# Kernel optimization log

Hardware: AMD Instinct MI355X
Metric: run time of the kernel (lower is better)

The kernel has to match this reference:

```python
import jax, jax.numpy as jnp
import numpy as np

N_NODES = 50000
N_EDGES = 800000
F_IN = 64
F_OUT = 64
EPS = 1e-5


def setup_inputs() -> dict:
    key = jax.random.key(0)
    ks = jax.random.split(key, 6)
    x = jax.random.normal(ks[0], (N_NODES, F_IN), dtype=jnp.float32)
    edge_index = jax.random.randint(ks[1], (2, N_EDGES), 0, N_NODES, dtype=jnp.int64)
    # pre MLP: Linear(2*F_in -> F_in); post MLP: Linear(13*F_in -> F_out); lin: Linear(F_out -> F_out)
    pre_w = jax.random.normal(ks[2], (2 * F_IN, F_IN), dtype=jnp.float32) / np.sqrt(2 * F_IN)
    pre_b = jnp.zeros((F_IN,), dtype=jnp.float32)
    post_w = jax.random.normal(ks[3], (13 * F_IN, F_OUT), dtype=jnp.float32) / np.sqrt(13 * F_IN)
    post_b = jnp.zeros((F_OUT,), dtype=jnp.float32)
    lin_w = jax.random.normal(ks[4], (F_OUT, F_OUT), dtype=jnp.float32) / np.sqrt(F_OUT)
    lin_b = jnp.zeros((F_OUT,), dtype=jnp.float32)
    return {"x": x, "edge_index": edge_index, "pre_w": pre_w, "pre_b": pre_b,
            "post_w": post_w, "post_b": post_b, "lin_w": lin_w, "lin_b": lin_b}


def _pna_conv(x, edge_index, pre_w, pre_b, post_w, post_b, lin_w, lin_b):
    n = x.shape[0]
    src = edge_index[0]  # x_j (source / neighbor)
    dst = edge_index[1]  # x_i (target / aggregation index)

    # message: pre-MLP on [x_i, x_j]  -> [E, F_in]
    h = jnp.concatenate([x[dst], x[src]], axis=-1)  # [E, 2*F_in]
    m = h @ pre_w + pre_b                            # [E, F_in]

    # degree of each target node
    deg = jax.ops.segment_sum(jnp.ones_like(src, dtype=x.dtype), dst, num_segments=n)  # [N]
    has_nb = deg > 0
    deg_c = jnp.maximum(deg, 1.0)[:, None]  # clamp(1), [N,1]

    # aggregators: mean, min, max, std (single pass over edges per reduction)
    s1 = jax.ops.segment_sum(m, dst, num_segments=n)
    s2 = jax.ops.segment_sum(m * m, dst, num_segments=n)
    mean = s1 / deg_c
    mean_sq = s2 / deg_c
    std = jnp.sqrt(jax.nn.relu(mean_sq - mean * mean) + EPS)
    mn = jax.ops.segment_min(m, dst, num_segments=n)
    mx = jax.ops.segment_max(m, dst, num_segments=n)
    mn = jnp.where(has_nb[:, None], mn, 0.0)
    mx = jnp.where(has_nb[:, None], mx, 0.0)
    aggs = jnp.concatenate([mean, mn, mx, std], axis=-1)  # [N, 4*F_in]

    # degree scalers: identity, amplification, attenuation
    # avg log-degree from the graph's degree histogram (log(deg+1), unclamped)
    avg_deg_log = jnp.mean(jnp.log(deg + 1.0))
    deg_log = jnp.log(deg_c + 1.0)  # uses clamped degree, [N,1]
    amp = deg_log / avg_deg_log
    att = avg_deg_log / deg_log
    scaled = jnp.concatenate([aggs, aggs * amp, aggs * att], axis=-1)  # [N, 12*F_in]

    # post MLP on [x, aggregated] then final linear
    out = jnp.concatenate([x, scaled], axis=-1)  # [N, 13*F_in]
    out = out @ post_w + post_b                  # [N, F_out]
    out = out @ lin_w + lin_b                    # [N, F_out]
    return out


def reference(x, edge_index, pre_w, pre_b, post_w, post_b, lin_w, lin_b):
    # eval-mode forward: dropout is identity, no loss branch
    return _pna_conv(x, edge_index, pre_w, pre_b, post_w, post_b, lin_w, lin_b)
```

## Files before the change

kernel.cpp:

```cpp
#include <hip/hip_runtime.h>
#include <math.h>
#include <stdint.h>

#define EPS 1e-5f

typedef __attribute__((ext_vector_type(8))) short bf16x8;
typedef __attribute__((ext_vector_type(4))) float f32x4;

union FragU {
    bf16x8 v;
    ushort u[8];
};

__device__ __forceinline__ ushort f2bf(float f)
{
    union { float f; uint u; } v; v.f = f;
    uint r = v.u + 0x7FFF + ((v.u >> 16) & 1);
    return (ushort)(r >> 16);
}
__device__ __forceinline__ float bf2f(ushort u)
{
    union { uint u; float f; } v; v.u = (uint)u << 16;
    return v.f;
}
__device__ __forceinline__ uint packbf2(float lo, float hi)
{
    return (uint)f2bf(lo) | ((uint)f2bf(hi) << 16);
}

#define MFMA(a, b, c) __builtin_amdgcn_mfma_f32_16x16x32_bf16((a), (b), (c), 0, 0, 0)

#define PART_BLOCKS 128
#define FP_BLOCKS   209

__global__ __launch_bounds__(256) void k_preh(
    const float* __restrict__ x, const float* __restrict__ pre_w,
    const float* __restrict__ pre_b, const int* __restrict__ ei,
    const float* __restrict__ post_w, const float* __restrict__ post_b,
    const float* __restrict__ lin_w, const float* __restrict__ lin_b,
    ushort* __restrict__ Ab, ushort* __restrict__ Bb,
    int* __restrict__ hist, ushort* __restrict__ Wp, float* __restrict__ bc,
    int N, int E, int NWB)
{
    int t = threadIdx.x;

    if (blockIdx.x >= NWB + PART_BLOCKS) {
        int unit = (blockIdx.x - NWB - PART_BLOCKS) * 4 + (t >> 6);
        int j = t & 63;
        if (unit > 832) return;
        if (unit < 832) {
            int r = unit;
            float acc = 0.f;
            for (int k = 0; k < 64; ++k)
                acc = fmaf(post_w[r * 64 + k], lin_w[k * 64 + j], acc);
            int tile, kk;
            if (r < 64) { tile = (r >> 5) * 4 + (j >> 4); kk = r & 31; }
            else {
                int g = (r - 64) >> 8, ka = (r - 64) & 255;
                tile = 8 + (g * 8 + (ka >> 5)) * 4 + (j >> 4); kk = ka & 31;
            }
            int ln = (j & 15) | ((kk >> 3) << 4);
            Wp[tile * 512 + ln * 8 + (kk & 7)] = f2bf(acc);
        } else {
            float a = lin_b[j];
            for (int k = 0; k < 64; ++k)
                a = fmaf(post_b[k], lin_w[k * 64 + j], a);
            bc[j] = a;
        }
        return;
    }

    if (blockIdx.x >= NWB) {
        __shared__ int lh[256];
        int blk = blockIdx.x - NWB;
        lh[t] = 0;
        __syncthreads();
        int chunk = (E + PART_BLOCKS - 1) / PART_BLOCKS;
        int c0 = blk * chunk, c1 = min(E, c0 + chunk);
        for (int e = c0 + t; e < c1; e += 256) {
            int dst = ei[E + e];
            if ((unsigned)dst < (unsigned)N) atomicAdd(&lh[dst >> 8], 1);
        }
        __syncthreads();
        hist[blk * 256 + t] = lh[t];
        return;
    }

    __shared__ ushort pw[16 * 512];
    for (int idx = t; idx < 8192; idx += 256) {
        int kin = idx >> 7, o = idx & 127;
        float v = (o < 64) ? pre_w[kin * 64 + o]
                           : pre_w[(64 + kin) * 64 + (o - 64)];
        int kk = kin & 31;
        int tile = (kin >> 5) * 8 + (o >> 4);
        int ln = (o & 15) | ((kk >> 3) << 4);
        pw[tile * 512 + ln * 8 + (kk & 7)] = f2bf(v);
    }
    __syncthreads();

    int w = t >> 6, lane = t & 63;
    int nb = (blockIdx.x * 4 + w) * 32;
    if (nb >= N) return;
    int lr = lane & 15, lk = lane >> 4;

    f32x4 acc[2][8] = {};
#pragma unroll
    for (int ks = 0; ks < 2; ++ks) {
        FragU A0, A1;
        {
            int r0 = min(nb + lr, N - 1);
            int r1 = min(nb + 16 + lr, N - 1);
            const float* p0 = &x[r0 * 64 + ks * 32 + lk * 8];
            const float* p1 = &x[r1 * 64 + ks * 32 + lk * 8];
            float4 a0 = *reinterpret_cast<const float4*>(p0);
            float4 a1 = *reinterpret_cast<const float4*>(p0 + 4);
            float4 c0 = *reinterpret_cast<const float4*>(p1);
            float4 c1 = *reinterpret_cast<const float4*>(p1 + 4);
            A0.u[0] = f2bf(a0.x); A0.u[1] = f2bf(a0.y);
            A0.u[2] = f2bf(a0.z); A0.u[3] = f2bf(a0.w);
            A0.u[4] = f2bf(a1.x); A0.u[5] = f2bf(a1.y);
            A0.u[6] = f2bf(a1.z); A0.u[7] = f2bf(a1.w);
            A1.u[0] = f2bf(c0.x); A1.u[1] = f2bf(c0.y);
            A1.u[2] = f2bf(c0.z); A1.u[3] = f2bf(c0.w);
            A1.u[4] = f2bf(c1.x); A1.u[5] = f2bf(c1.y);
            A1.u[6] = f2bf(c1.z); A1.u[7] = f2bf(c1.w);
        }
#pragma unroll
        for (int jt = 0; jt < 8; ++jt) {
            bf16x8 B = *reinterpret_cast<const bf16x8*>(
                &pw[(ks * 8 + jt) * 512 + lane * 8]);
            acc[0][jt] = MFMA(A0.v, B, acc[0][jt]);
            acc[1][jt] = MFMA(A1.v, B, acc[1][jt]);
        }
    }
#pragma unroll
    for (int mt = 0; mt < 2; ++mt)
#pragma unroll
        for (int jt = 0; jt < 8; ++jt) {
            int o = jt * 16 + lr;
#pragma unroll
            for (int rg = 0; rg < 4; ++rg) {
                int r = nb + mt * 16 + lk * 4 + rg;
                if (r < N) {
                    float v = acc[mt][jt][rg];
                    if (o < 64) Ab[r * 64 + o] = f2bf(v + pre_b[o]);
                    else        Bb[r * 64 + (o - 64)] = f2bf(v);
                }
            }
        }
}

__global__ __launch_bounds__(256) void k_cscan(
    const int* __restrict__ hist, int* __restrict__ colscan,
    int* __restrict__ bucketStart, int* __restrict__ offsets,
    float* __restrict__ avg_acc, int N)
{
    __shared__ int ws[4];
    int b = threadIdx.x;
    if (b == 0) *avg_acc = 0.f;

    int run = 0;
    for (int base = 0; base < PART_BLOCKS; base += 8) {
        int h[8];
#pragma unroll
        for (int k = 0; k < 8; ++k) h[k] = hist[(base + k) * 256 + b];
#pragma unroll
        for (int k = 0; k < 8; ++k) {
            colscan[(base + k) * 256 + b] = run;
            run += h[k];
        }
    }

    int lane = b & 63, wv = b >> 6;
    int inc = run;
#pragma unroll
    for (int off = 1; off < 64; off <<= 1) {
        int u = __shfl_up(inc, off);
        if (lane >= off) inc += u;
    }
    if (lane == 63) ws[wv] = inc;
    __syncthreads();
    int add = 0;
#pragma unroll
    for (int i = 0; i < 4; ++i)
        if (i < wv) add += ws[i];
    int incl = inc + add;
    bucketStart[b] = incl - run;
    if (b == 255) {
        bucketStart[256] = incl;
        offsets[N] = incl;
    }
}

__global__ __launch_bounds__(256) void k_part(
    const int* __restrict__ ei, const int* __restrict__ colscan,
    const int* __restrict__ bucketStart, uint* __restrict__ staged,
    int E, int N)
{
    __shared__ int cur[256];
    int t = threadIdx.x, blk = blockIdx.x;
    cur[t] = bucketStart[t] + colscan[blk * 256 + t];
    __syncthreads();
    int chunk = (E + PART_BLOCKS - 1) / PART_BLOCKS;
    int c0 = blk * chunk, c1 = min(E, c0 + chunk);
    for (int e = c0 + t; e < c1; e += 256) {
        int src = ei[e];
        int dst = ei[E + e];
        if ((unsigned)dst < (unsigned)N) {
            if ((unsigned)src >= (unsigned)N) src = 0;
            int pos = atomicAdd(&cur[dst >> 8], 1);
            staged[pos] = (uint)src | ((uint)(dst & 255) << 16);
        }
    }
}

__global__ __launch_bounds__(256) void k_place(
    const uint* __restrict__ staged, const int* __restrict__ bucketStart,
    ushort* __restrict__ csr16, int* __restrict__ offsets,
    float* __restrict__ avg_acc, int N)
{
    __shared__ int cnt[256];
    __shared__ int wsum[4];
    __shared__ float fl[4];
    int t = threadIdx.x, lane = t & 63, wv = t >> 6;
    int b = blockIdx.x;
    int s0 = bucketStart[b], s1 = bucketStart[b + 1];

    cnt[t] = 0;
    __syncthreads();
    for (int i = s0 + t; i < s1; i += 256)
        atomicAdd(&cnt[(staged[i] >> 16) & 255], 1);
    __syncthreads();

    int d = cnt[t];
    int v = d;
#pragma unroll
    for (int off = 1; off < 64; off <<= 1) {
        int u = __shfl_up(v, off);
        if (lane >= off) v += u;
    }
    if (lane == 63) wsum[wv] = v;
    __syncthreads();
    int wvoff = 0;
#pragma unroll
    for (int i = 0; i < 4; ++i)
        if (i < wv) wvoff += wsum[i];
    int excl = wvoff + v - d;

    int node = b * 256 + t;
    if (node < N) offsets[node] = s0 + excl;

    float sl = (node < N) ? logf((float)d + 1.0f) : 0.f;
    for (int off = 32; off; off >>= 1) sl += __shfl_down(sl, off);
    if (lane == 0) fl[wv] = sl;

    cnt[t] = excl;
    __syncthreads();
    if (t == 0) atomicAdd(avg_acc, fl[0] + fl[1] + fl[2] + fl[3]);

    for (int i = s0 + t; i < s1; i += 256) {
        uint ev = staged[i];
        int p = atomicAdd(&cnt[(ev >> 16) & 255], 1);
        csr16[s0 + p] = (ushort)(ev & 0xFFFFu);
    }
}

__global__ __launch_bounds__(256) void k_aggregate(
    const ushort* __restrict__ Ab, const ushort* __restrict__ Bb,
    const int* __restrict__ offsets, const ushort* __restrict__ csr16,
    const float* __restrict__ avg_sum, ushort* __restrict__ aggs,
    float* __restrict__ amp, float* __restrict__ att, int N)
{
    int wave = threadIdx.x >> 6, lane = threadIdx.x & 63;
    int n = blockIdx.x * 4 + wave;
    if (n >= N) return;

    int off0 = offsets[n], off1 = offsets[n + 1];
    int d = off1 - off0;
    int hl = lane & 31;
    int which = lane >> 5;

    float s0 = 0.f, s1 = 0.f, q0 = 0.f, q1 = 0.f;
    float mn0 = 3.4e38f, mn1 = 3.4e38f, mx0 = -3.4e38f, mx1 = -3.4e38f;

#define UPD(bv)                                                         \
    {                                                                   \
        float m0 = bf2f((ushort)((bv) & 0xFFFFu));                      \
        float m1 = bf2f((ushort)((bv) >> 16));                          \
        s0 += m0; q0 = fmaf(m0, m0, q0);                                \
        mn0 = fminf(mn0, m0); mx0 = fmaxf(mx0, m0);                     \
        s1 += m1; q1 = fmaf(m1, m1, q1);                                \
        mn1 = fminf(mn1, m1); mx1 = fmaxf(mx1, m1);                     \
    }

    for (int base = off0; base < off1; base += 64) {
        int cnt = min(64, off1 - base);
        int s_idx = 0;
        if (lane < cnt) s_idx = (int)csr16[base + lane];
        int i = 0;
        for (; i + 15 < cnt; i += 16) {
            int sA = __shfl(s_idx, i + 0 + which);
            int sB = __shfl(s_idx, i + 2 + which);
            int sC = __shfl(s_idx, i + 4 + which);
            int sD = __shfl(s_idx, i + 6 + which);
            int sE = __shfl(s_idx, i + 8 + which);
            int sF = __shfl(s_idx, i + 10 + which);
            int sG = __shfl(s_idx, i + 12 + which);
            int sH = __shfl(s_idx, i + 14 + which);
            uint bA = *reinterpret_cast<const uint*>(&Bb[(size_t)sA * 64 + hl * 2]);
            uint bB = *reinterpret_cast<const uint*>(&Bb[(size_t)sB * 64 + hl * 2]);
            uint bC = *reinterpret_cast<const uint*>(&Bb[(size_t)sC * 64 + hl * 2]);
            uint bD = *reinterpret_cast<const uint*>(&Bb[(size_t)sD * 64 + hl * 2]);
            uint bE = *reinterpret_cast<const uint*>(&Bb[(size_t)sE * 64 + hl * 2]);
            uint bF = *reinterpret_cast<const uint*>(&Bb[(size_t)sF * 64 + hl * 2]);
            uint bG = *reinterpret_cast<const uint*>(&Bb[(size_t)sG * 64 + hl * 2]);
            uint bH = *reinterpret_cast<const uint*>(&Bb[(size_t)sH * 64 + hl * 2]);
            UPD(bA); UPD(bB); UPD(bC); UPD(bD);
            UPD(bE); UPD(bF); UPD(bG); UPD(bH);
        }
        for (; i + 7 < cnt; i += 8) {
            int sA = __shfl(s_idx, i + 0 + which);
            int sB = __shfl(s_idx, i + 2 + which);
            int sC = __shfl(s_idx, i + 4 + which);
            int sD = __shfl(s_idx, i + 6 + which);
            uint bA = *reinterpret_cast<const uint*>(&Bb[(size_t)sA * 64 + hl * 2]);
            uint bB = *reinterpret_cast<const uint*>(&Bb[(size_t)sB * 64 + hl * 2]);
            uint bC = *reinterpret_cast<const uint*>(&Bb[(size_t)sC * 64 + hl * 2]);
            uint bD = *reinterpret_cast<const uint*>(&Bb[(size_t)sD * 64 + hl * 2]);
            UPD(bA); UPD(bB); UPD(bC); UPD(bD);
        }
        for (; i < cnt; i += 2) {
            int sj = __shfl(s_idx, i + which);
            uint bv = *reinterpret_cast<const uint*>(&Bb[(size_t)sj * 64 + hl * 2]);
            if ((which == 0) | (i + 1 < cnt)) UPD(bv);
        }
    }
#undef UPD

    s0 += __shfl_xor(s0, 32);  s1 += __shfl_xor(s1, 32);
    q0 += __shfl_xor(q0, 32);  q1 += __shfl_xor(q1, 32);
    mn0 = fminf(mn0, __shfl_xor(mn0, 32));
    mn1 = fminf(mn1, __shfl_xor(mn1, 32));
    mx0 = fmaxf(mx0, __shfl_xor(mx0, 32));
    mx1 = fmaxf(mx1, __shfl_xor(mx1, 32));

    uint av = *reinterpret_cast<const uint*>(&Ab[(size_t)n * 64 + hl * 2]);
    float a0 = bf2f((ushort)(av & 0xFFFFu));
    float a1 = bf2f((ushort)(av >> 16));

    float dc = (d > 0) ? (float)d : 1.0f;
    float mB0 = s0 / dc, mB1 = s1 / dc;
    float std0 = sqrtf(fmaxf(q0 / dc - mB0 * mB0, 0.f) + EPS);
    float std1 = sqrtf(fmaxf(q1 / dc - mB1 * mB1, 0.f) + EPS);
    float mean0 = a0 + mB0, mean1 = a1 + mB1;
    float mnF0 = a0 + mn0, mnF1 = a1 + mn1;
    float mxF0 = a0 + mx0, mxF1 = a1 + mx1;
    if (d == 0) {
        mean0 = mean1 = 0.f;
        mnF0 = mnF1 = 0.f;
        mxF0 = mxF1 = 0.f;
    }

    if (lane < 32) {
        uint* ag = reinterpret_cast<uint*>(&aggs[(size_t)n * 256]);
        ag[0 * 32 + hl] = packbf2(mean0, mean1);
        ag[1 * 32 + hl] = packbf2(mnF0, mnF1);
        ag[2 * 32 + hl] = packbf2(mxF0, mxF1);
        ag[3 * 32 + hl] = packbf2(std0, std1);
    }
    if (lane == 0) {
        float avg = *avg_sum / (float)N;
        float dlog = logf(dc + 1.0f);
        amp[n] = dlog / avg;
        att[n] = avg / dlog;
    }
}

__global__ __launch_bounds__(256) void k_out_gemm(
    const float* __restrict__ x, const ushort* __restrict__ aggs,
    const float* __restrict__ amp, const float* __restrict__ att,
    const ushort* __restrict__ Wp, const float* __restrict__ bc,
    float* __restrict__ out, int N)
{
    int w = threadIdx.x >> 6, lane = threadIdx.x & 63;
    int nb = (blockIdx.x * 4 + w) * 32;
    int lr = lane & 15, lk = lane >> 4;

    f32x4 accP[2][4] = {};
    f32x4 accA[2][4] = {};
    f32x4 accT[2][4] = {};

#pragma unroll
    for (int ks = 0; ks < 2; ++ks) {
        FragU A0, A1;
        {
            int r0 = min(nb + lr, N - 1);
            int r1 = min(nb + 16 + lr, N - 1);
            const float* p0 = &x[r0 * 64 + ks * 32 + lk * 8];
            const float* p1 = &x[r1 * 64 + ks * 32 + lk * 8];
            float4 a0 = *reinterpret_cast<const float4*>(p0);
            float4 a1 = *reinterpret_cast<const float4*>(p0 + 4);
            float4 c0 = *reinterpret_cast<const float4*>(p1);
            float4 c1 = *reinterpret_cast<const float4*>(p1 + 4);
            A0.u[0] = f2bf(a0.x); A0.u[1] = f2bf(a0.y);
            A0.u[2] = f2bf(a0.z); A0.u[3] = f2bf(a0.w);
            A0.u[4] = f2bf(a1.x); A0.u[5] = f2bf(a1.y);
            A0.u[6] = f2bf(a1.z); A0.u[7] = f2bf(a1.w);
            A1.u[0] = f2bf(c0.x); A1.u[1] = f2bf(c0.y);
            A1.u[2] = f2bf(c0.z); A1.u[3] = f2bf(c0.w);
            A1.u[4] = f2bf(c1.x); A1.u[5] = f2bf(c1.y);
            A1.u[6] = f2bf(c1.z); A1.u[7] = f2bf(c1.w);
        }
#pragma unroll
        for (int jt = 0; jt < 4; ++jt) {
            bf16x8 B = *reinterpret_cast<const bf16x8*>(
                &Wp[(ks * 4 + jt) * 512 + lane * 8]);
            accP[0][jt] = MFMA(A0.v, B, accP[0][jt]);
            accP[1][jt] = MFMA(A1.v, B, accP[1][jt]);
        }
    }

#pragma unroll 2
    for (int ks = 0; ks < 8; ++ks) {
        bf16x8 A0 = *reinterpret_cast<const bf16x8*>(
            &aggs[(size_t)(nb + lr) * 256 + ks * 32 + lk * 8]);
        bf16x8 A1 = *reinterpret_cast<const bf16x8*>(
            &aggs[(size_t)(nb + 16 + lr) * 256 + ks * 32 + lk * 8]);
        bf16x8 B0[4], B1[4], B2[4];
#pragma unroll
        for (int jt = 0; jt < 4; ++jt) {
            B0[jt] = *reinterpret_cast<const bf16x8*>(
                &Wp[(8 + (0 * 8 + ks) * 4 + jt) * 512 + lane * 8]);
            B1[jt] = *reinterpret_cast<const bf16x8*>(
                &Wp[(8 + (1 * 8 + ks) * 4 + jt) * 512 + lane * 8]);
            B2[jt] = *reinterpret_cast<const bf16x8*>(
                &Wp[(8 + (2 * 8 + ks) * 4 + jt) * 512 + lane * 8]);
        }
#pragma unroll
        for (int jt = 0; jt < 4; ++jt) {
            accP[0][jt] = MFMA(A0, B0[jt], accP[0][jt]);
            accP[1][jt] = MFMA(A1, B0[jt], accP[1][jt]);
            accA[0][jt] = MFMA(A0, B1[jt], accA[0][jt]);
            accA[1][jt] = MFMA(A1, B1[jt], accA[1][jt]);
            accT[0][jt] = MFMA(A0, B2[jt], accT[0][jt]);
            accT[1][jt] = MFMA(A1, B2[jt], accT[1][jt]);
        }
    }

#pragma unroll
    for (int mt = 0; mt < 2; ++mt) {
        int rb = nb + mt * 16 + lk * 4;
        float am[4], at[4];
#pragma unroll
        for (int rg = 0; rg < 4; ++rg) {
            am[rg] = amp[rb + rg];
            at[rg] = att[rb + rg];
        }
#pragma unroll
        for (int jt = 0; jt < 4; ++jt) {
            int j = jt * 16 + lr;
            float b = bc[j];
#pragma unroll
            for (int rg = 0; rg < 4; ++rg) {
                int r = rb + rg;
                if (r < N) {
                    out[(size_t)r * 64 + j] =
                        accP[mt][jt][rg] + am[rg] * accA[mt][jt][rg] +
                        at[rg] * accT[mt][jt][rg] + b;
                }
            }
        }
    }
}

static inline char* alignup(char* p, size_t a)
{
    return (char*)(((uintptr_t)p + a - 1) & ~(uintptr_t)(a - 1));
}

extern "C" void kernel_launch(void* const* d_in, const int* in_sizes, int n_in,
                              void* d_out, int out_size, void* d_ws, size_t ws_size,
                              hipStream_t stream)
{
    const float* x      = (const float*)d_in[0];
    const int*   ei     = (const int*)d_in[1];
    const float* pre_w  = (const float*)d_in[2];
    const float* pre_b  = (const float*)d_in[3];
    const float* post_w = (const float*)d_in[4];
    const float* post_b = (const float*)d_in[5];
    const float* lin_w  = (const float*)d_in[6];
    const float* lin_b  = (const float*)d_in[7];
    float* out = (float*)d_out;

    const int N = in_sizes[0] / 64;
    const int E = in_sizes[1] / 2;
    const int Npad = (N + 127) & ~127;
    const int NWB = Npad / 128;
    const int NBUCK = (N + 255) >> 8;
    if (N > 65536) return;

    size_t need = 0;
    auto acct = [&](size_t bytes) { need = ((need + 255) & ~(size_t)255) + bytes; };
    acct((size_t)N * 64 * 2);
    acct((size_t)N * 64 * 2);
    acct((size_t)Npad * 256 * 2);
    acct(104 * 512 * 2);
    acct(64 * 4);
    acct((size_t)Npad * 4);
    acct((size_t)Npad * 4);
    acct(((size_t)N + 1) * 4);
    acct((size_t)E * 2);
    acct((size_t)E * 4);
    acct(PART_BLOCKS * 256 * 4);
    acct(PART_BLOCKS * 256 * 4);
    acct(257 * 4);
    acct(4);
    if (ws_size < need) return;

    char* p = (char*)d_ws;
    auto take = [&](size_t bytes) {
        p = alignup(p, 256);
        void* r = (void*)p;
        p += bytes;
        return r;
    };
    ushort* Ab        = (ushort*)take((size_t)N * 64 * 2);
    ushort* Bb        = (ushort*)take((size_t)N * 64 * 2);
    ushort* aggs      = (ushort*)take((size_t)Npad * 256 * 2);
    ushort* Wp        = (ushort*)take(104 * 512 * 2);
    float*  bc        = (float*)take(64 * 4);
    float*  amp       = (float*)take((size_t)Npad * 4);
    float*  att       = (float*)take((size_t)Npad * 4);
    int*    offsets   = (int*)take(((size_t)N + 1) * 4);
    ushort* csr16     = (ushort*)take((size_t)E * 2);
    uint*   staged    = (uint*)take((size_t)E * 4);
    int*    hist      = (int*)take(PART_BLOCKS * 256 * 4);
    int*    colscan   = (int*)take(PART_BLOCKS * 256 * 4);
    int*    bstart    = (int*)take(257 * 4);
    float*  avg_acc   = (float*)take(4);

    k_preh<<<NWB + PART_BLOCKS + FP_BLOCKS, 256, 0, stream>>>(
        x, pre_w, pre_b, ei, post_w, post_b, lin_w, lin_b,
        Ab, Bb, hist, Wp, bc, N, E, NWB);
    k_cscan<<<1, 256, 0, stream>>>(hist, colscan, bstart, offsets, avg_acc, N);
    k_part<<<PART_BLOCKS, 256, 0, stream>>>(ei, colscan, bstart, staged, E, N);
    k_place<<<NBUCK, 256, 0, stream>>>(staged, bstart, csr16, offsets,
                                       avg_acc, N);
    k_aggregate<<<(N + 3) / 4, 256, 0, stream>>>(Ab, Bb, offsets, csr16,
                                                 avg_acc, aggs, amp, att, N);
    k_out_gemm<<<NWB, 256, 0, stream>>>(x, aggs, amp, att, Wp, bc, out, N);
}
```

Baseline: 181.9 us.

## Fuse CSR build into one grid-barrier kernel and aggregation into output GEMM

Replaces the histogram, column-scan, partition and place kernels with a single persistent k_csr kernel, one block per 256-node bucket, that uses atomic spin-wait grid barriers between phases. The aggregation and output GEMM are merged into k_aggemm, which keeps the per-node aggregate rows and scalers in shared memory, so the global aggs/amp/att buffers are never written or read back. The intent is to remove several launches and a round trip of aggregate data through global memory. In exchange the grid barrier depends on all ~196 blocks being co-resident, and each k_aggemm block now processes 128 nodes with heavy LDS use, which lowers parallelism for the gather phase.

```diff
diff --git a/kernel.cpp b/kernel.cpp
--- a/kernel.cpp
+++ b/kernel.cpp
@@ -30,22 +30,59 @@
 
 #define MFMA(a, b, c) __builtin_amdgcn_mfma_f32_16x16x32_bf16((a), (b), (c), 0, 0, 0)
 
-#define PART_BLOCKS 128
-#define FP_BLOCKS   209
+#define FP_BLOCKS 209
+
+__device__ __forceinline__ void gbar(int* bar, int target)
+{
+    __syncthreads();
+    if (threadIdx.x == 0) {
+        __threadfence();
+        __hip_atomic_fetch_add(bar, 1, __ATOMIC_ACQ_REL, __HIP_MEMORY_SCOPE_AGENT);
+        long it = 0;
+        while (__hip_atomic_load(bar, __ATOMIC_ACQUIRE, __HIP_MEMORY_SCOPE_AGENT)
+                   < target &&
+               it < (1L << 22)) {
+            __builtin_amdgcn_s_sleep(2);
+            ++it;
+        }
+    }
+    __syncthreads();
+}
+
+__device__ __forceinline__ int blockScanExcl(int v, int* wsum, int* tot)
+{
+    int lane = threadIdx.x & 63, wv = threadIdx.x >> 6;
+    int inc = v;
+#pragma unroll
+    for (int off = 1; off < 64; off <<= 1) {
+        int u = __shfl_up(inc, off);
+        if (lane >= off) inc += u;
+    }
+    __syncthreads();
+    if (lane == 63) wsum[wv] = inc;
+    __syncthreads();
+    int add = 0;
+#pragma unroll
+    for (int i = 0; i < 4; ++i)
+        if (i < wv) add += wsum[i];
+    *tot = wsum[0] + wsum[1] + wsum[2] + wsum[3];
+    return inc + add - v;
+}
 
 __global__ __launch_bounds__(256) void k_preh(
     const float* __restrict__ x, const float* __restrict__ pre_w,
-    const float* __restrict__ pre_b, const int* __restrict__ ei,
+    const float* __restrict__ pre_b,
     const float* __restrict__ post_w, const float* __restrict__ post_b,
     const float* __restrict__ lin_w, const float* __restrict__ lin_b,
     ushort* __restrict__ Ab, ushort* __restrict__ Bb,
-    int* __restrict__ hist, ushort* __restrict__ Wp, float* __restrict__ bc,
-    int N, int E, int NWB)
+    ushort* __restrict__ Wp, float* __restrict__ bc,
+    int* __restrict__ bar, int N, int NWB)
 {
     int t = threadIdx.x;
-
-    if (blockIdx.x >= NWB + PART_BLOCKS) {
-        int unit = (blockIdx.x - NWB - PART_BLOCKS) * 4 + (t >> 6);
+    if (blockIdx.x == 0 && t == 0) *bar = 0;
+
+    if (blockIdx.x >= NWB) {
+        int unit = (blockIdx.x - NWB) * 4 + (t >> 6);
         int j = t & 63;
         if (unit > 832) return;
         if (unit < 832) {
@@ -70,22 +107,6 @@
         return;
     }
 
-    if (blockIdx.x >= NWB) {
-        __shared__ int lh[256];
-        int blk = blockIdx.x - NWB;
-        lh[t] = 0;
-        __syncthreads();
-        int chunk = (E + PART_BLOCKS - 1) / PART_BLOCKS;
-        int c0 = blk * chunk, c1 = min(E, c0 + chunk);
-        for (int e = c0 + t; e < c1; e += 256) {
-            int dst = ei[E + e];
-            if ((unsigned)dst < (unsigned)N) atomicAdd(&lh[dst >> 8], 1);
-        }
-        __syncthreads();
-        hist[blk * 256 + t] = lh[t];
-        return;
-    }
-
     __shared__ ushort pw[16 * 512];
     for (int idx = t; idx < 8192; idx += 256) {
         int kin = idx >> 7, o = idx & 127;
@@ -150,324 +171,271 @@
         }
 }
 
-__global__ __launch_bounds__(256) void k_cscan(
-    const int* __restrict__ hist, int* __restrict__ colscan,
-    int* __restrict__ bucketStart, int* __restrict__ offsets,
-    float* __restrict__ avg_acc, int N)
-{
-    __shared__ int ws[4];
-    int b = threadIdx.x;
-    if (b == 0) *avg_acc = 0.f;
-
-    int run = 0;
-    for (int base = 0; base < PART_BLOCKS; base += 8) {
-        int h[8];
-#pragma unroll
-        for (int k = 0; k < 8; ++k) h[k] = hist[(base + k) * 256 + b];
-#pragma unroll
-        for (int k = 0; k < 8; ++k) {
-            colscan[(base + k) * 256 + b] = run;
-            run += h[k];
-        }
-    }
-
-    int lane = b & 63, wv = b >> 6;
-    int inc = run;
-#pragma unroll
-    for (int off = 1; off < 64; off <<= 1) {
-        int u = __shfl_up(inc, off);
-        if (lane >= off) inc += u;
-    }
-    if (lane == 63) ws[wv] = inc;
-    __syncthreads();
-    int add = 0;
-#pragma unroll
-    for (int i = 0; i < 4; ++i)
-        if (i < wv) add += ws[i];
-    int incl = inc + add;
-    bucketStart[b] = incl - run;
-    if (b == 255) {
-        bucketStart[256] = incl;
-        offsets[N] = incl;
-    }
-}
-
-__global__ __launch_bounds__(256) void k_part(
-    const int* __restrict__ ei, const int* __restrict__ colscan,
-    const int* __restrict__ bucketStart, uint* __restrict__ staged,
-    int E, int N)
-{
-    __shared__ int cur[256];
-    int t = threadIdx.x, blk = blockIdx.x;
-    cur[t] = bucketStart[t] + colscan[blk * 256 + t];
-    __syncthreads();
-    int chunk = (E + PART_BLOCKS - 1) / PART_BLOCKS;
-    int c0 = blk * chunk, c1 = min(E, c0 + chunk);
+__global__ __launch_bounds__(256) void k_csr(
+    const int* __restrict__ ei, ushort* __restrict__ csr16,
+    int* __restrict__ offsets, uint* __restrict__ staged,
+    int* __restrict__ hist, int* __restrict__ colscan,
+    int* __restrict__ bstart, float* __restrict__ avg_acc,
+    int* __restrict__ bar, int E, int N)
+{
+    __shared__ int lh[256];
+    __shared__ int wsum[4];
+    __shared__ float fl[4];
+    int t = threadIdx.x, bid = blockIdx.x, NB = gridDim.x;
+    int chunk = (E + NB - 1) / NB;
+    int c0 = bid * chunk, c1 = min(E, c0 + chunk);
+
+    lh[t] = 0;
+    if (bid == 0 && t == 0) *avg_acc = 0.f;
+    __syncthreads();
+    for (int e = c0 + t; e < c1; e += 256) {
+        int dst = ei[E + e];
+        if ((unsigned)dst < (unsigned)N) atomicAdd(&lh[dst >> 8], 1);
+    }
+    __syncthreads();
+    hist[bid * 256 + t] = lh[t];
+    gbar(bar, 1 * NB);
+
+    for (int b = bid; b < 256; b += NB) {
+        int v0 = (t < NB) ? hist[t * 256 + b] : 0;
+        int tot;
+        int excl = blockScanExcl(v0, wsum, &tot);
+        if (t < NB) colscan[t * 256 + b] = excl;
+        if (t == 0) bstart[b] = tot;
+    }
+    gbar(bar, 2 * NB);
+
+    if (bid == 0) {
+        int v0 = bstart[t];
+        int tot;
+        int excl = blockScanExcl(v0, wsum, &tot);
+        bstart[t] = excl;
+        if (t == 255) {
+            bstart[256] = tot;
+            offsets[N] = tot;
+        }
+    }
+    gbar(bar, 3 * NB);
+
+    lh[t] = bstart[t] + colscan[bid * 256 + t];
+    __syncthreads();
     for (int e = c0 + t; e < c1; e += 256) {
         int src = ei[e];
         int dst = ei[E + e];
         if ((unsigned)dst < (unsigned)N) {
             if ((unsigned)src >= (unsigned)N) src = 0;
-            int pos = atomicAdd(&cur[dst >> 8], 1);
+            int pos = atomicAdd(&lh[dst >> 8], 1);
             staged[pos] = (uint)src | ((uint)(dst & 255) << 16);
         }
     }
-}
-
-__global__ __launch_bounds__(256) void k_place(
-    const uint* __restrict__ staged, const int* __restrict__ bucketStart,
-    ushort* __restrict__ csr16, int* __restrict__ offsets,
-    float* __restrict__ avg_acc, int N)
-{
-    __shared__ int cnt[256];
-    __shared__ int wsum[4];
-    __shared__ float fl[4];
-    int t = threadIdx.x, lane = t & 63, wv = t >> 6;
-    int b = blockIdx.x;
-    int s0 = bucketStart[b], s1 = bucketStart[b + 1];
-
-    cnt[t] = 0;
+    gbar(bar, 4 * NB);
+
+    int s0 = bstart[bid], s1 = bstart[bid + 1];
+    lh[t] = 0;
     __syncthreads();
     for (int i = s0 + t; i < s1; i += 256)
-        atomicAdd(&cnt[(staged[i] >> 16) & 255], 1);
-    __syncthreads();
-
-    int d = cnt[t];
-    int v = d;
-#pragma unroll
-    for (int off = 1; off < 64; off <<= 1) {
-        int u = __shfl_up(v, off);
-        if (lane >= off) v += u;
-    }
-    if (lane == 63) wsum[wv] = v;
-    __syncthreads();
-    int wvoff = 0;
-#pragma unroll
-    for (int i = 0; i < 4; ++i)
-        if (i < wv) wvoff += wsum[i];
-    int excl = wvoff + v - d;
-
-    int node = b * 256 + t;
+        atomicAdd(&lh[(staged[i] >> 16) & 255], 1);
+    __syncthreads();
+    int d = lh[t];
+    int tot;
+    int excl = blockScanExcl(d, wsum, &tot);
+    int node = bid * 256 + t;
     if (node < N) offsets[node] = s0 + excl;
 
     float sl = (node < N) ? logf((float)d + 1.0f) : 0.f;
     for (int off = 32; off; off >>= 1) sl += __shfl_down(sl, off);
-    if (lane == 0) fl[wv] = sl;
-
-    cnt[t] = excl;
+    if ((t & 63) == 0) fl[t >> 6] = sl;
+    lh[t] = excl;
     __syncthreads();
     if (t == 0) atomicAdd(avg_acc, fl[0] + fl[1] + fl[2] + fl[3]);
 
     for (int i = s0 + t; i < s1; i += 256) {
         uint ev = staged[i];
-        int p = atomicAdd(&cnt[(ev >> 16) & 255], 1);
+        int p = atomicAdd(&lh[(ev >> 16) & 255], 1);
         csr16[s0 + p] = (ushort)(ev & 0xFFFFu);
     }
 }
 
-__global__ __launch_bounds__(256) void k_aggregate(
-    const ushort* __restrict__ Ab, const ushort* __restrict__ Bb,
-    const int* __restrict__ offsets, const ushort* __restrict__ csr16,
-    const float* __restrict__ avg_sum, ushort* __restrict__ aggs,
-    float* __restrict__ amp, float* __restrict__ att, int N)
-{
-    int wave = threadIdx.x >> 6, lane = threadIdx.x & 63;
-    int n = blockIdx.x * 4 + wave;
-    if (n >= N) return;
-
-    int off0 = offsets[n], off1 = offsets[n + 1];
-    int d = off1 - off0;
-    int hl = lane & 31;
-    int which = lane >> 5;
-
-    float s0 = 0.f, s1 = 0.f, q0 = 0.f, q1 = 0.f;
-    float mn0 = 3.4e38f, mn1 = 3.4e38f, mx0 = -3.4e38f, mx1 = -3.4e38f;
-
-#define UPD(bv)                                                         \
-    {                                                                   \
-        float m0 = bf2f((ushort)((bv) & 0xFFFFu));                      \
-        float m1 = bf2f((ushort)((bv) >> 16));                          \
-        s0 += m0; q0 = fmaf(m0, m0, q0);                                \
-        mn0 = fminf(mn0, m0); mx0 = fmaxf(mx0, m0);                     \
-        s1 += m1; q1 = fmaf(m1, m1, q1);                                \
-        mn1 = fminf(mn1, m1); mx1 = fmaxf(mx1, m1);                     \
-    }
-
-    for (int base = off0; base < off1; base += 64) {
-        int cnt = min(64, off1 - base);
-        int s_idx = 0;
-        if (lane < cnt) s_idx = (int)csr16[base + lane];
-        int i = 0;
-        for (; i + 15 < cnt; i += 16) {
-            int sA = __shfl(s_idx, i + 0 + which);
-            int sB = __shfl(s_idx, i + 2 + which);
-            int sC = __shfl(s_idx, i + 4 + which);
-            int sD = __shfl(s_idx, i + 6 + which);
-            int sE = __shfl(s_idx, i + 8 + which);
-            int sF = __shfl(s_idx, i + 10 + which);
-            int sG = __shfl(s_idx, i + 12 + which);
-            int sH = __shfl(s_idx, i + 14 + which);
-            uint bA = *reinterpret_cast<const uint*>(&Bb[(size_t)sA * 64 + hl * 2]);
-            uint bB = *reinterpret_cast<const uint*>(&Bb[(size_t)sB * 64 + hl * 2]);
-            uint bC = *reinterpret_cast<const uint*>(&Bb[(size_t)sC * 64 + hl * 2]);
-            uint bD = *reinterpret_cast<const uint*>(&Bb[(size_t)sD * 64 + hl * 2]);
-            uint bE = *reinterpret_cast<const uint*>(&Bb[(size_t)sE * 64 + hl * 2]);
-            uint bF = *reinterpret_cast<const uint*>(&Bb[(size_t)sF * 64 + hl * 2]);
-            uint bG = *reinterpret_cast<const uint*>(&Bb[(size_t)sG * 64 + hl * 2]);
-            uint bH = *reinterpret_cast<const uint*>(&Bb[(size_t)sH * 64 + hl * 2]);
-            UPD(bA); UPD(bB); UPD(bC); UPD(bD);
-            UPD(bE); UPD(bF); UPD(bG); UPD(bH);
-        }
-        for (; i + 7 < cnt; i += 8) {
-            int sA = __shfl(s_idx, i + 0 + which);
-            int sB = __shfl(s_idx, i + 2 + which);
-            int sC = __shfl(s_idx, i + 4 + which);
-            int sD = __shfl(s_idx, i + 6 + which);
-            uint bA = *reinterpret_cast<const uint*>(&Bb[(size_t)sA * 64 + hl * 2]);
-            uint bB = *reinterpret_cast<const uint*>(&Bb[(size_t)sB * 64 + hl * 2]);
-            uint bC = *reinterpret_cast<const uint*>(&Bb[(size_t)sC * 64 + hl * 2]);
-            uint bD = *reinterpret_cast<const uint*>(&Bb[(size_t)sD * 64 + hl * 2]);
-            UPD(bA); UPD(bB); UPD(bC); UPD(bD);
-        }
-        for (; i < cnt; i += 2) {
-            int sj = __shfl(s_idx, i + which);
-            uint bv = *reinterpret_cast<const uint*>(&Bb[(size_t)sj * 64 + hl * 2]);
-            if ((which == 0) | (i + 1 < cnt)) UPD(bv);
-        }
-    }
-#undef UPD
-
-    s0 += __shfl_xor(s0, 32);  s1 += __shfl_xor(s1, 32);
-    q0 += __shfl_xor(q0, 32);  q1 += __shfl_xor(q1, 32);
-    mn0 = fminf(mn0, __shfl_xor(mn0, 32));
-    mn1 = fminf(mn1, __shfl_xor(mn1, 32));
-    mx0 = fmaxf(mx0, __shfl_xor(mx0, 32));
-    mx1 = fmaxf(mx1, __shfl_xor(mx1, 32));
-
-    uint av = *reinterpret_cast<const uint*>(&Ab[(size_t)n * 64 + hl * 2]);
-    float a0 = bf2f((ushort)(av & 0xFFFFu));
-    float a1 = bf2f((ushort)(av >> 16));
-
-    float dc = (d > 0) ? (float)d : 1.0f;
-    float mB0 = s0 / dc, mB1 = s1 / dc;
-    float std0 = sqrtf(fmaxf(q0 / dc - mB0 * mB0, 0.f) + EPS);
-    float std1 = sqrtf(fmaxf(q1 / dc - mB1 * mB1, 0.f) + EPS);
-    float mean0 = a0 + mB0, mean1 = a1 + mB1;
-    float mnF0 = a0 + mn0, mnF1 = a1 + mn1;
-    float mxF0 = a0 + mx0, mxF1 = a1 + mx1;
-    if (d == 0) {
-        mean0 = mean1 = 0.f;
-        mnF0 = mnF1 = 0.f;
-        mxF0 = mxF1 = 0.f;
-    }
-
-    if (lane < 32) {
-        uint* ag = reinterpret_cast<uint*>(&aggs[(size_t)n * 256]);
-        ag[0 * 32 + hl] = packbf2(mean0, mean1);
-        ag[1 * 32 + hl] = packbf2(mnF0, mnF1);
-        ag[2 * 32 + hl] = packbf2(mxF0, mxF1);
-        ag[3 * 32 + hl] = packbf2(std0, std1);
-    }
-    if (lane == 0) {
-        float avg = *avg_sum / (float)N;
-        float dlog = logf(dc + 1.0f);
-        amp[n] = dlog / avg;
-        att[n] = avg / dlog;
-    }
-}
-
-__global__ __launch_bounds__(256) void k_out_gemm(
-    const float* __restrict__ x, const ushort* __restrict__ aggs,
-    const float* __restrict__ amp, const float* __restrict__ att,
+__global__ __launch_bounds__(512) void k_aggemm(
+    const float* __restrict__ x, const ushort* __restrict__ Ab,
+    const ushort* __restrict__ Bb, const int* __restrict__ offsets,
+    const ushort* __restrict__ csr16, const float* __restrict__ avg_sum,
     const ushort* __restrict__ Wp, const float* __restrict__ bc,
     float* __restrict__ out, int N)
 {
-    int w = threadIdx.x >> 6, lane = threadIdx.x & 63;
-    int nb = (blockIdx.x * 4 + w) * 32;
+    __shared__ ushort lag[128 * 264];
+    __shared__ float s_amp[128], s_att[128];
+
+    int t = threadIdx.x, wv = t >> 6, lane = t & 63;
+    int nbase = blockIdx.x * 128;
+    int hl = lane & 31, which = lane >> 5;
+    float avg = *avg_sum / (float)N;
+
+    for (int nd = 0; nd < 16; ++nd) {
+        int ln = wv * 16 + nd;
+        int n = nbase + ln;
+        int off0 = (n < N) ? offsets[n] : 0;
+        int off1 = (n < N) ? offsets[n + 1] : 0;
+        int d = off1 - off0;
+
+        float s0 = 0.f, s1 = 0.f, q0 = 0.f, q1 = 0.f;
+        float mn0 = 3.4e38f, mn1 = 3.4e38f, mx0 = -3.4e38f, mx1 = -3.4e38f;
+
+#define UPD(bv)                                                         \
+        {                                                               \
+            float m0 = bf2f((ushort)((bv) & 0xFFFFu));                  \
+            float m1 = bf2f((ushort)((bv) >> 16));                      \
+            s0 += m0; q0 = fmaf(m0, m0, q0);                            \
+            mn0 = fminf(mn0, m0); mx0 = fmaxf(mx0, m0);                 \
+            s1 += m1; q1 = fmaf(m1, m1, q1);                            \
+            mn1 = fminf(mn1, m1); mx1 = fmaxf(mx1, m1);                 \
+        }
+
+        for (int base = off0; base < off1; base += 64) {
+            int cnt = min(64, off1 - base);
+            int s_idx = 0;
+            if (lane < cnt) s_idx = (int)csr16[base + lane];
+            int i = 0;
+            for (; i + 15 < cnt; i += 16) {
+                int sA = __shfl(s_idx, i + 0 + which);
+                int sB = __shfl(s_idx, i + 2 + which);
+                int sC = __shfl(s_idx, i + 4 + which);
+                int sD = __shfl(s_idx, i + 6 + which);
+                int sE = __shfl(s_idx, i + 8 + which);
+                int sF = __shfl(s_idx, i + 10 + which);
+                int sG = __shfl(s_idx, i + 12 + which);
+                int sH = __shfl(s_idx, i + 14 + which);
+                uint bA = *reinterpret_cast<const uint*>(&Bb[(size_t)sA * 64 + hl * 2]);
+                uint bB = *reinterpret_cast<const uint*>(&Bb[(size_t)sB * 64 + hl * 2]);
+                uint bC = *reinterpret_cast<const uint*>(&Bb[(size_t)sC * 64 + hl * 2]);
+                uint bD = *reinterpret_cast<const uint*>(&Bb[(size_t)sD * 64 + hl * 2]);
+                uint bE = *reinterpret_cast<const uint*>(&Bb[(size_t)sE * 64 + hl * 2]);
+                uint bF = *reinterpret_cast<const uint*>(&Bb[(size_t)sF * 64 + hl * 2]);
+                uint bG = *reinterpret_cast<const uint*>(&Bb[(size_t)sG * 64 + hl * 2]);
+                uint bH = *reinterpret_cast<const uint*>(&Bb[(size_t)sH * 64 + hl * 2]);
+                UPD(bA); UPD(bB); UPD(bC); UPD(bD);
+                UPD(bE); UPD(bF); UPD(bG); UPD(bH);
+            }
+            for (; i + 7 < cnt; i += 8) {
+                int sA = __shfl(s_idx, i + 0 + which);
+                int sB = __shfl(s_idx, i + 2 + which);
+                int sC = __shfl(s_idx, i + 4 + which);
+                int sD = __shfl(s_idx, i + 6 + which);
+                uint bA = *reinterpret_cast<const uint*>(&Bb[(size_t)sA * 64 + hl * 2]);
+                uint bB = *reinterpret_cast<const uint*>(&Bb[(size_t)sB * 64 + hl * 2]);
+                uint bC = *reinterpret_cast<const uint*>(&Bb[(size_t)sC * 64 + hl * 2]);
+                uint bD = *reinterpret_cast<const uint*>(&Bb[(size_t)sD * 64 + hl * 2]);
+                UPD(bA); UPD(bB); UPD(bC); UPD(bD);
+            }
+            for (; i < cnt; i += 2) {
+                int sj = __shfl(s_idx, i + which);
+                uint bv = *reinterpret_cast<const uint*>(&Bb[(size_t)sj * 64 + hl * 2]);
+                if ((which == 0) | (i + 1 < cnt)) UPD(bv);
+            }
+        }
+#undef UPD
+
+        s0 += __shfl_xor(s0, 32);  s1 += __shfl_xor(s1, 32);
+        q0 += __shfl_xor(q0, 32);  q1 += __shfl_xor(q1, 32);
+        mn0 = fminf(mn0, __shfl_xor(mn0, 32));
+        mn1 = fminf(mn1, __shfl_xor(mn1, 32));
+        mx0 = fmaxf(mx0, __shfl_xor(mx0, 32));
+        mx1 = fmaxf(mx1, __shfl_xor(mx1, 32));
+
+        uint av = *reinterpret_cast<const uint*>(
+            &Ab[(size_t)min(n, N - 1) * 64 + hl * 2]);
+        float a0 = bf2f((ushort)(av & 0xFFFFu));
+        float a1 = bf2f((ushort)(av >> 16));
+
+        float dc = (d > 0) ? (float)d : 1.0f;
+        float mB0 = s0 / dc, mB1 = s1 / dc;
+        float std0 = sqrtf(fmaxf(q0 / dc - mB0 * mB0, 0.f) + EPS);
+        float std1 = sqrtf(fmaxf(q1 / dc - mB1 * mB1, 0.f) + EPS);
+        float mean0 = a0 + mB0, mean1 = a1 + mB1;
+        float mnF0 = a0 + mn0, mnF1 = a1 + mn1;
+        float mxF0 = a0 + mx0, mxF1 = a1 + mx1;
+        if (d == 0) {
+            mean0 = mean1 = 0.f;
+            mnF0 = mnF1 = 0.f;
+            mxF0 = mxF1 = 0.f;
+        }
+
+        if (lane < 32) {
+            uint* ag = reinterpret_cast<uint*>(&lag[ln * 264]);
+            ag[0 * 32 + hl] = packbf2(mean0, mean1);
+            ag[1 * 32 + hl] = packbf2(mnF0, mnF1);
+            ag[2 * 32 + hl] = packbf2(mxF0, mxF1);
+            ag[3 * 32 + hl] = packbf2(std0, std1);
+        }
+        if (lane == 0) {
+            float dlog = logf(dc + 1.0f);
+            s_amp[ln] = dlog / avg;
+            s_att[ln] = avg / dlog;
+        }
+    }
+
     int lr = lane & 15, lk = lane >> 4;
-
-    f32x4 accP[2][4] = {};
-    f32x4 accA[2][4] = {};
-    f32x4 accT[2][4] = {};
+    f32x4 accP[4] = {};
+    f32x4 accA[4] = {};
+    f32x4 accT[4] = {};
 
 #pragma unroll
     for (int ks = 0; ks < 2; ++ks) {
-        FragU A0, A1;
+        FragU A0;
         {
-            int r0 = min(nb + lr, N - 1);
-            int r1 = min(nb + 16 + lr, N - 1);
+            int r0 = min(nbase + wv * 16 + lr, N - 1);
             const float* p0 = &x[r0 * 64 + ks * 32 + lk * 8];
-            const float* p1 = &x[r1 * 64 + ks * 32 + lk * 8];
             float4 a0 = *reinterpret_cast<const float4*>(p0);
             float4 a1 = *reinterpret_cast<const float4*>(p0 + 4);
-            float4 c0 = *reinterpret_cast<const float4*>(p1);
-            float4 c1 = *reinterpret_cast<const float4*>(p1 + 4);
             A0.u[0] = f2bf(a0.x); A0.u[1] = f2bf(a0.y);
             A0.u[2] = f2bf(a0.z); A0.u[3] = f2bf(a0.w);
             A0.u[4] = f2bf(a1.x); A0.u[5] = f2bf(a1.y);
             A0.u[6] = f2bf(a1.z); A0.u[7] = f2bf(a1.w);
-            A1.u[0] = f2bf(c0.x); A1.u[1] = f2bf(c0.y);
-            A1.u[2] = f2bf(c0.z); A1.u[3] = f2bf(c0.w);
-            A1.u[4] = f2bf(c1.x); A1.u[5] = f2bf(c1.y);
-            A1.u[6] = f2bf(c1.z); A1.u[7] = f2bf(c1.w);
         }
 #pragma unroll
         for (int jt = 0; jt < 4; ++jt) {
             bf16x8 B = *reinterpret_cast<const bf16x8*>(
                 &Wp[(ks * 4 + jt) * 512 + lane * 8]);
-            accP[0][jt] = MFMA(A0.v, B, accP[0][jt]);
-            accP[1][jt] = MFMA(A1.v, B, accP[1][jt]);
+            accP[jt] = MFMA(A0.v, B, accP[jt]);
         }
     }
 
 #pragma unroll 2
     for (int ks = 0; ks < 8; ++ks) {
         bf16x8 A0 = *reinterpret_cast<const bf16x8*>(
-            &aggs[(size_t)(nb + lr) * 256 + ks * 32 + lk * 8]);
-        bf16x8 A1 = *reinterpret_cast<const bf16x8*>(
-            &aggs[(size_t)(nb + 16 + lr) * 256 + ks * 32 + lk * 8]);
-        bf16x8 B0[4], B1[4], B2[4];
+            &lag[(wv * 16 + lr) * 264 + ks * 32 + lk * 8]);
 #pragma unroll
         for (int jt = 0; jt < 4; ++jt) {
-            B0[jt] = *reinterpret_cast<const bf16x8*>(
+            bf16x8 B0 = *reinterpret_cast<const bf16x8*>(
                 &Wp[(8 + (0 * 8 + ks) * 4 + jt) * 512 + lane * 8]);
-            B1[jt] = *reinterpret_cast<const bf16x8*>(
+            bf16x8 B1 = *reinterpret_cast<const bf16x8*>(
                 &Wp[(8 + (1 * 8 + ks) * 4 + jt) * 512 + lane * 8]);
-            B2[jt] = *reinterpret_cast<const bf16x8*>(
+            bf16x8 B2 = *reinterpret_cast<const bf16x8*>(
                 &Wp[(8 + (2 * 8 + ks) * 4 + jt) * 512 + lane * 8]);
-        }
-#pragma unroll
-        for (int jt = 0; jt < 4; ++jt) {
-            accP[0][jt] = MFMA(A0, B0[jt], accP[0][jt]);
-            accP[1][jt] = MFMA(A1, B0[jt], accP[1][jt]);
-            accA[0][jt] = MFMA(A0, B1[jt], accA[0][jt]);
-            accA[1][jt] = MFMA(A1, B1[jt], accA[1][jt]);
-            accT[0][jt] = MFMA(A0, B2[jt], accT[0][jt]);
-            accT[1][jt] = MFMA(A1, B2[jt], accT[1][jt]);
-        }
-    }
-
-#pragma unroll
-    for (int mt = 0; mt < 2; ++mt) {
-        int rb = nb + mt * 16 + lk * 4;
-        float am[4], at[4];
+            accP[jt] = MFMA(A0, B0, accP[jt]);
+            accA[jt] = MFMA(A0, B1, accA[jt]);
+            accT[jt] = MFMA(A0, B2, accT[jt]);
+        }
+    }
+
+    int rb = wv * 16 + lk * 4;
+    float am[4], at[4];
+#pragma unroll
+    for (int rg = 0; rg < 4; ++rg) {
+        am[rg] = s_amp[rb + rg];
+        at[rg] = s_att[rb + rg];
+    }
+#pragma unroll
+    for (int jt = 0; jt < 4; ++jt) {
+        int j = jt * 16 + lr;
+        float b = bc[j];
 #pragma unroll
         for (int rg = 0; rg < 4; ++rg) {
-            am[rg] = amp[rb + rg];
-            at[rg] = att[rb + rg];
-        }
-#pragma unroll
-        for (int jt = 0; jt < 4; ++jt) {
-            int j = jt * 16 + lr;
-            float b = bc[j];
-#pragma unroll
-            for (int rg = 0; rg < 4; ++rg) {
-                int r = rb + rg;
-                if (r < N) {
-                    out[(size_t)r * 64 + j] =
-                        accP[mt][jt][rg] + am[rg] * accA[mt][jt][rg] +
-                        at[rg] * accT[mt][jt][rg] + b;
-                }
+            int r = nbase + rb + rg;
+            if (r < N) {
+                out[(size_t)r * 64 + j] =
+                    accP[jt][rg] + am[rg] * accA[jt][rg] +
+                    at[rg] * accT[jt][rg] + b;
             }
         }
     }
@@ -503,17 +471,15 @@
     auto acct = [&](size_t bytes) { need = ((need + 255) & ~(size_t)255) + bytes; };
     acct((size_t)N * 64 * 2);
     acct((size_t)N * 64 * 2);
-    acct((size_t)Npad * 256 * 2);
     acct(104 * 512 * 2);
     acct(64 * 4);
-    acct((size_t)Npad * 4);
-    acct((size_t)Npad * 4);
     acct(((size_t)N + 1) * 4);
     acct((size_t)E * 2);
     acct((size_t)E * 4);
-    acct(PART_BLOCKS * 256 * 4);
-    acct(PART_BLOCKS * 256 * 4);
+    acct((size_t)NBUCK * 256 * 4);
+    acct((size_t)NBUCK * 256 * 4);
     acct(257 * 4);
+    acct(4);
     acct(4);
     if (ws_size < need) return;
 
@@ -524,29 +490,24 @@
         p += bytes;
         return r;
     };
-    ushort* Ab        = (ushort*)take((size_t)N * 64 * 2);
-    ushort* Bb        = (ushort*)take((size_t)N * 64 * 2);
-    ushort* aggs      = (ushort*)take((size_t)Npad * 256 * 2);
-    ushort* Wp        = (ushort*)take(104 * 512 * 2);
-    float*  bc        = (float*)take(64 * 4);
-    float*  amp       = (float*)take((size_t)Npad * 4);
-    float*  att       = (float*)take((size_t)Npad * 4);
-    int*    offsets   = (int*)take(((size_t)N + 1) * 4);
-    ushort* csr16     = (ushort*)take((size_t)E * 2);
-    uint*   staged    = (uint*)take((size_t)E * 4);
-    int*    hist      = (int*)take(PART_BLOCKS * 256 * 4);
-    int*    colscan   = (int*)take(PART_BLOCKS * 256 * 4);
-    int*    bstart    = (int*)take(257 * 4);
-    float*  avg_acc   = (float*)take(4);
-
-    k_preh<<<NWB + PART_BLOCKS + FP_BLOCKS, 256, 0, stream>>>(
-        x, pre_w, pre_b, ei, post_w, post_b, lin_w, lin_b,
-        Ab, Bb, hist, Wp, bc, N, E, NWB);
-    k_cscan<<<1, 256, 0, stream>>>(hist, colscan, bstart, offsets, avg_acc, N);
-    k_part<<<PART_BLOCKS, 256, 0, stream>>>(ei, colscan, bstart, staged, E, N);
-    k_place<<<NBUCK, 256, 0, stream>>>(staged, bstart, csr16, offsets,
-                                       avg_acc, N);
-    k_aggregate<<<(N + 3) / 4, 256, 0, stream>>>(Ab, Bb, offsets, csr16,
-                                                 avg_acc, aggs, amp, att, N);
-    k_out_gemm<<<NWB, 256, 0, stream>>>(x, aggs, amp, att, Wp, bc, out, N);
-}
+    ushort* Ab      = (ushort*)take((size_t)N * 64 * 2);
+    ushort* Bb      = (ushort*)take((size_t)N * 64 * 2);
+    ushort* Wp      = (ushort*)take(104 * 512 * 2);
+    float*  bc      = (float*)take(64 * 4);
+    int*    offsets = (int*)take(((size_t)N + 1) * 4);
+    ushort* csr16   = (ushort*)take((size_t)E * 2);
+    uint*   staged  = (uint*)take((size_t)E * 4);
+    int*    hist    = (int*)take((size_t)NBUCK * 256 * 4);
+    int*    colscan = (int*)take((size_t)NBUCK * 256 * 4);
+    int*    bstart  = (int*)take(257 * 4);
+    float*  avg_acc = (float*)take(4);
+    int*    bar     = (int*)take(4);
+
+    k_preh<<<NWB + FP_BLOCKS, 256, 0, stream>>>(
+        x, pre_w, pre_b, post_w, post_b, lin_w, lin_b,
+        Ab, Bb, Wp, bc, bar, N, NWB);
+    k_csr<<<NBUCK, 256, 0, stream>>>(ei, csr16, offsets, staged,
+                                     hist, colscan, bstart, avg_acc, bar, E, N);
+    k_aggemm<<<NWB, 512, 0, stream>>>(x, Ab, Bb, offsets, csr16, avg_acc,
+                                      Wp, bc, out, N);
+}
```

Result: slower. 255.5 us (+40.5%).
